# Performance work log

Hardware: AMD Instinct MI355X
Metric: run time of the kernel (lower is better)

The kernel has to match this reference:

```python
import jax, jax.numpy as jnp
import numpy as np

AMBIENT = [2, 2, 2]
DEGREES = [a + 1 for a in AMBIENT]          # coords per projective factor
N_COORDS = sum(DEGREES)                      # 9
STARTS = np.concatenate([[0], np.cumsum(DEGREES)[:-1]])
CONST_MULT = 1.0
CLIP = 1.0e6


def _get_real_imag_of_prod(cp):
    """cp: complex [B, n]. Returns (real [B, n(n+1)/2], imag [B, n(n-1)/2]).
    Matches TF boolean_mask(transpose(...)) ordering: row-major (b, a) with b<=a;
    real = (XX+YY)[x, b, a] (symmetric), imag = +XY_YX[x, b, a] for b<a."""
    X, Y = jnp.real(cp), jnp.imag(cp)
    XX_YY = jnp.einsum('xa,xb->xab', X, X) + jnp.einsum('xa,xb->xab', Y, Y)
    XY = jnp.einsum('xa,xb->xab', X, Y)
    XY_YX = XY - XY.transpose(0, 2, 1)      # antisymmetric
    n = cp.shape[1]
    iu = jnp.triu_indices(n)                # incl. diagonal
    su = jnp.triu_indices(n, 1)             # strict upper
    real = XX_YY[:, iu[0], iu[1]]
    imag = XY_YX[:, su[0], su[1]]
    return real, imag


def _bihom(points):
    """points: complex [B, N_COORDS] -> real [B, 729] section products / kappa."""
    B = points.shape[0]
    kappas_prod = jnp.ones((B,), points.real.dtype)
    it_r = it_i = None
    for i, (s, d) in enumerate(zip(STARTS, DEGREES)):
        cp = points[:, s:s + d]
        kappas_prod = kappas_prod * jnp.sum(jnp.abs(cp) ** 2, axis=-1)
        r, im = _get_real_imag_of_prod(cp)
        if i == 0:
            it_r, it_i = r, im
        else:
            new_r = jnp.concatenate([
                jnp.einsum('bi,bj->bij', it_r, r).reshape(B, -1),
                -jnp.einsum('bi,bj->bij', it_i, im).reshape(B, -1)], axis=1)
            new_i = jnp.concatenate([
                jnp.einsum('bi,bj->bij', it_r, im).reshape(B, -1),
                -jnp.einsum('bi,bj->bij', it_i, r).reshape(B, -1)], axis=1)
            it_r, it_i = new_r, new_i
    sec = jnp.concatenate([it_r, it_i], axis=-1)
    return sec / kappas_prod[:, None]


def _tower(h, W1, b1, W2, b2, W3, b3, Wf):
    # Dense layers with square activation, then log|.| into bias-free final Dense
    h = (h @ W1 + b1) ** 2
    h = (h @ W2 + b2) ** 2
    h = (h @ W3 + b3) ** 2
    return jnp.log(jnp.abs(h)) @ Wf


def setup_inputs() -> dict:
    key = jax.random.key(0)
    ks = jax.random.split(key, 16)
    B = 32768
    s = 0.05
    inp = {
        'x':   jax.random.normal(ks[0], (B, 2 * N_COORDS), jnp.float32),
        'W1a': jax.random.normal(ks[1], (729, 1024), jnp.float32) * s,
        'b1a': jax.random.normal(ks[2], (1024,), jnp.float32) * s,
        'W2a': jax.random.normal(ks[3], (1024, 1024), jnp.float32) * s,
        'b2a': jax.random.normal(ks[4], (1024,), jnp.float32) * s,
        'W3a': jax.random.normal(ks[5], (1024, 1), jnp.float32) * s,
        'b3a': jax.random.normal(ks[6], (1,), jnp.float32) * s,
        'Wfa': jnp.ones((1, 1), jnp.float32),
        'W1b': jax.random.normal(ks[7], (729, 1024), jnp.float32) * s,
        'b1b': jax.random.normal(ks[8], (1024,), jnp.float32) * s,
        'W2b': jax.random.normal(ks[9], (1024, 1024), jnp.float32) * s,
        'b2b': jax.random.normal(ks[10], (1024,), jnp.float32) * s,
        'W3b': jax.random.normal(ks[11], (1024, 1), jnp.float32) * s,
        'b3b': jax.random.normal(ks[12], (1,), jnp.float32) * s,
        'Wfb': jnp.ones((1, 1), jnp.float32),
    }
    return inp


def reference(x, W1a, b1a, W2a, b2a, W3a, b3a, Wfa,
              W1b, b1b, W2b, b2b, W3b, b3b, Wfb):
    points = jax.lax.complex(x[:, :N_COORDS], x[:, N_COORDS:])
    feats = _bihom(points)                     # [B, 729]
    out = _tower(feats, W1a, b1a, W2a, b2a, W3a, b3a, Wfa) \
        - _tower(feats, W1b, b1b, W2b, b2b, W3b, b3b, Wfb)
    return CONST_MULT * jnp.clip(out, -CLIP, CLIP)
```

## Files before the change

kernel.cpp:

```cpp
#include <hip/hip_runtime.h>

typedef unsigned short u16;
typedef unsigned int u32;
typedef __attribute__((ext_vector_type(8))) short bf16x8;
typedef __attribute__((ext_vector_type(4))) float f32x4;

__device__ __forceinline__ u16 f2bf(float x){
  unsigned u = __builtin_bit_cast(unsigned, x);
  unsigned r = (u + 0x7FFFu + ((u >> 16) & 1u)) >> 16;
  return (u16)r;
}
__device__ __forceinline__ float bf2f(u16 h){
  unsigned u = ((unsigned)h) << 16;
  return __builtin_bit_cast(float, u);
}

__device__ __forceinline__ void gld_lds16(const void* g, void* l){
  __builtin_amdgcn_global_load_lds((const __attribute__((address_space(1))) void*)g,
                                   (__attribute__((address_space(3))) void*)l,
                                   16, 0, 0);
}

__global__ void wconv_kernel(const float* __restrict__ W0, u16* __restrict__ Th0, int K0p,
                             const float* __restrict__ W1, u16* __restrict__ Th1, int K1p,
                             const float* __restrict__ W2, u16* __restrict__ Th2, int K2p,
                             const float* __restrict__ W3, u16* __restrict__ Th3, int K3p)
{
  __shared__ float t[32][33];
  int z = blockIdx.z;
  const float* W = z==0 ? W0 : z==1 ? W1 : z==2 ? W2 : W3;
  u16* Th = z==0 ? Th0 : z==1 ? Th1 : z==2 ? Th2 : Th3;
  int Kpad = z==0 ? K0p : z==1 ? K1p : z==2 ? K2p : K3p;
  int K = (Kpad == 768) ? 729 : 1024;
  int k0 = blockIdx.x * 32;
  if (k0 >= Kpad) return;
  int n0 = blockIdx.y * 32;
  int tx = threadIdx.x & 31, ty = threadIdx.x >> 5;
#pragma unroll
  for (int j = 0; j < 4; j++){
    int k = k0 + ty + j*8;
    float v = (k < K) ? W[(size_t)k*1024 + (n0 + tx)] : 0.f;
    t[ty + j*8][tx] = v;
  }
  __syncthreads();
#pragma unroll
  for (int j = 0; j < 4; j++){
    int n = n0 + ty + j*8;
    int k = k0 + tx;
    size_t idx = (size_t)n*Kpad + k;
    Th[idx] = f2bf(t[tx][ty + j*8]);
  }
}

__global__ void feats_kernel(const float* __restrict__ x,
                             u16* __restrict__ fh,
                             int row0)
{
  __shared__ float cC[8][28];
  __shared__ float tA[8][81];
  __shared__ float tB[8][12];
  __shared__ float ivk[8];
  const int tid = threadIdx.x;
  const int lrow0 = blockIdx.x * 8;
  if (tid < 8){
    const float* xr = x + (size_t)(row0 + lrow0 + tid) * 18;
    float kk = 1.f;
#pragma unroll
    for (int f = 0; f < 3; f++){
      float xa = xr[3*f+0], xb = xr[3*f+1], xc = xr[3*f+2];
      float ya = xr[9+3*f+0], yb = xr[9+3*f+1], yc = xr[9+3*f+2];
      int bse = f * 9;
      cC[tid][bse+0] = xa*xa + ya*ya;
      cC[tid][bse+1] = xa*xb + ya*yb;
      cC[tid][bse+2] = xa*xc + ya*yc;
      cC[tid][bse+3] = xb*xb + yb*yb;
      cC[tid][bse+4] = xb*xc + yb*yc;
      cC[tid][bse+5] = xc*xc + yc*yc;
      cC[tid][bse+6] = xa*yb - xb*ya;
      cC[tid][bse+7] = xa*yc - xc*ya;
      cC[tid][bse+8] = xb*yc - xc*yb;
      kk *= (xa*xa+ya*ya + xb*xb+yb*yb + xc*xc+yc*yc);
    }
    ivk[tid] = 1.f / kk;
#pragma unroll
    for (int j = 0; j < 6; j++) tB[tid][j] = cC[tid][18+j];
#pragma unroll
    for (int j = 0; j < 3; j++) tB[tid][6+j] = cC[tid][24+j];
  }
  __syncthreads();
#pragma unroll 1
  for (int e = tid; e < 648; e += 256){
    int r = e / 81;
    int k = e - r*81;
    const float* cc = cC[r];
    float val;
    if (k < 36)      {               val =   cc[k/6]     * cc[9  + k%6]; }
    else if (k < 45) { int u = k-36; val = -(cc[6 + u/3] * cc[15 + u%3]); }
    else if (k < 63) { int u = k-45; val =   cc[u/3]     * cc[15 + u%3]; }
    else             { int u = k-63; val = -(cc[6 + u/6] * cc[9  + u%6]); }
    tA[r][k] = val;
  }
  __syncthreads();
#pragma unroll 1
  for (int jj = 0; jj < 3; jj++){
    int o = jj*256 + tid;
    int idxA = 0, idxB = 0; float sgn = 0.f;
    if (o < 270)      {              idxA = o/6;      idxB = o - (o/6)*6; sgn =  1.f; }
    else if (o < 378) { int t = o-270; idxA = 45 + t/3; idxB = 6 + t%3;   sgn = -1.f; }
    else if (o < 513) { int t = o-378; idxA = t/3;      idxB = 6 + t%3;   sgn =  1.f; }
    else if (o < 729) { int t = o-513; idxA = 45 + t/6; idxB = t%6;       sgn = -1.f; }
#pragma unroll
    for (int r = 0; r < 8; r++){
      float v = sgn * tA[r][idxA] * tB[r][idxB] * ivk[r];
      size_t oi = (size_t)(lrow0 + r) * 768 + o;
      fh[oi] = f2bf(v);
    }
  }
}

#define GEMM_SMEM_BYTES (2*16384*2 + 4*256*4)

#define STAGE_A(BUF)  do{ u16* _a = sA + (BUF)*8192; \
    gld_lds16(gAh0, _a + wave*1024); gld_lds16(gAh1, _a + wave*1024 + 512); \
    gAh0 += 32; gAh1 += 32; }while(0)
#define STAGE_B(BUF) do{ u16* _b = sB + (BUF)*8192; \
    gld_lds16(gBh0, _b + wave*1024); gld_lds16(gBh1, _b + wave*1024 + 512); \
    gBh0 += 32; gBh1 += 32; }while(0)

#define BARRIER()  asm volatile("s_barrier" ::: "memory")
#define LGKM0()    asm volatile("s_waitcnt lgkmcnt(0)" ::: "memory")

#define CLUSTER(A, O, B) do{ \
    __builtin_amdgcn_s_setprio(1); \
    _Pragma("unroll") for (int m_ = 0; m_ < 4; m_++) \
      _Pragma("unroll") for (int n_ = 0; n_ < 4; n_++) \
        acc[(O)+m_][n_] = __builtin_amdgcn_mfma_f32_16x16x32_bf16((A)[m_], (B)[n_], acc[(O)+m_][n_], 0, 0, 0); \
    __builtin_amdgcn_s_setprio(0); \
  }while(0)

template<int MODE>
__global__ __launch_bounds__(512, 1) void gemm_k(
    const u16* __restrict__ Ahi,
    const u16* __restrict__ Bhi,
    const float* __restrict__ bias,
    u16* __restrict__ Oh,
    const float* __restrict__ W3, float* __restrict__ P, int Pstride,
    int K)
{
  extern __shared__ __align__(16) u16 smem[];
  u16* sA = smem;
  u16* sB = smem + 16384;
  float* rowsum = (float*)(smem + 32768);

  const int nwg = gridDim.x;
  const int qq = nwg >> 3;
  const int wg = (nwg & 7) ? (int)blockIdx.x
                           : ((blockIdx.x & 7) * qq + (blockIdx.x >> 3));
  const int nb = wg & 3;
  const int mb = wg >> 2;

  const int tid = threadIdx.x;
  const int wave = tid >> 6, lane = tid & 63;
  const int wm = wave >> 2, wn = wave & 3;

  const int l4 = lane >> 2, ls = lane & 3;
  const int fsw  = (l4 >> 1) & 3;
  const int koff = ((ls ^ fsw) << 3);

  const u16* gAh0 = Ahi + (size_t)(mb*256 + wave*32 + l4) * K + koff;
  const u16* gAh1 = gAh0 + (size_t)16 * K;
  const u16* gBh0 = Bhi + (size_t)(nb*256 + wave*32 + l4) * K + koff;
  const u16* gBh1 = gBh0 + (size_t)16 * K;

  const int r16 = lane & 15, g = lane >> 4;
  const int fr   = (r16 >> 1) & 3;
  const int slot = ((g ^ fr) << 3);

  f32x4 acc[8][4];
#pragma unroll
  for (int m = 0; m < 8; m++)
#pragma unroll
    for (int n = 0; n < 4; n++)
      acc[m][n] = (f32x4){0.f, 0.f, 0.f, 0.f};

  const int NT = K >> 5;
  STAGE_A(0); STAGE_B(0);
  asm volatile("s_waitcnt vmcnt(0)\n\ts_barrier" ::: "memory");

#pragma unroll 1
  for (int t = 0; t < NT; ++t){
    const int cur = t & 1, nxt = cur ^ 1;
    const u16* pA = sA + cur*8192;
    const u16* pB = sB + cur*8192;
    const bool pf = (t + 1 < NT);
    bf16x8 ah[8], bh[4];

#pragma unroll
    for (int n = 0; n < 4; n++) bh[n] = *(const bf16x8*)(pB + (wn*64 + n*16 + r16)*32 + slot);
#pragma unroll
    for (int m = 0; m < 4; m++) ah[m] = *(const bf16x8*)(pA + (wm*128 + m*16 + r16)*32 + slot);
    if (pf){ STAGE_A(nxt); }
    BARRIER(); LGKM0();
    CLUSTER(ah, 0, bh);
    BARRIER();

#pragma unroll
    for (int m = 0; m < 4; m++) ah[4+m] = *(const bf16x8*)(pA + (wm*128 + (4+m)*16 + r16)*32 + slot);
    if (pf){ STAGE_B(nxt); }
    BARRIER(); LGKM0();
    CLUSTER(ah+4, 4, bh);
    if (pf){
      asm volatile("s_waitcnt vmcnt(0)\n\ts_barrier" ::: "memory");
    } else {
      BARRIER();
    }
  }

  if constexpr (MODE == 0){
#pragma unroll
    for (int n = 0; n < 4; n++){
      int col = nb*256 + wn*64 + n*16 + r16;
      float bv = bias[col];
#pragma unroll
      for (int m = 0; m < 8; m++){
        int rbase = mb*256 + wm*128 + m*16 + g*4;
#pragma unroll
        for (int q = 0; q < 4; q++){
          float val = acc[m][n][q] + bv;
          val = val * val;
          size_t oi = (size_t)(rbase + q) * 1024 + col;
          Oh[oi] = f2bf(val);
        }
      }
    }
  } else {
    float w3v[4], bv[4];
#pragma unroll
    for (int n = 0; n < 4; n++){
      int col = nb*256 + wn*64 + n*16 + r16;
      w3v[n] = W3[col];
      bv[n]  = bias[col];
    }
    float rp[8][4];
#pragma unroll
    for (int m = 0; m < 8; m++)
#pragma unroll
      for (int q = 0; q < 4; q++)
        rp[m][q] = 0.f;
#pragma unroll
    for (int m = 0; m < 8; m++)
#pragma unroll
      for (int n = 0; n < 4; n++)
#pragma unroll
        for (int q = 0; q < 4; q++){
          float v = acc[m][n][q] + bv[n];
          rp[m][q] += v * v * w3v[n];
        }
#pragma unroll
    for (int m = 0; m < 8; m++)
#pragma unroll
      for (int q = 0; q < 4; q++){
        float s = rp[m][q];
        s += __shfl_xor(s, 1); s += __shfl_xor(s, 2);
        s += __shfl_xor(s, 4); s += __shfl_xor(s, 8);
        rp[m][q] = s;
      }
    if (r16 == 0){
#pragma unroll
      for (int m = 0; m < 8; m++)
#pragma unroll
        for (int q = 0; q < 4; q++)
          rowsum[wn*256 + wm*128 + m*16 + g*4 + q] = rp[m][q];
    }
    __syncthreads();
    if (tid < 256){
      float s = rowsum[tid] + rowsum[256 + tid] + rowsum[512 + tid] + rowsum[768 + tid];
      P[(size_t)nb * Pstride + mb*256 + tid] = s;
    }
  }
}

__global__ void finalize_kernel(const float* __restrict__ Pa, const float* __restrict__ Pb,
                                int Pstride,
                                const float* __restrict__ b3a, const float* __restrict__ Wfa,
                                const float* __restrict__ b3b, const float* __restrict__ Wfb,
                                float* __restrict__ out, int row0, int Rc)
{
  int r = blockIdx.x * 256 + threadIdx.x;
  if (r >= Rc) return;
  float sa = b3a[0], sb = b3b[0];
#pragma unroll
  for (int j = 0; j < 4; j++){
    sa += Pa[(size_t)j * Pstride + r];
    sb += Pb[(size_t)j * Pstride + r];
  }
  float ta = 2.f * logf(fabsf(sa)) * Wfa[0];
  float tb = 2.f * logf(fabsf(sb)) * Wfb[0];
  float o = ta - tb;
  o = fminf(fmaxf(o, -1000000.f), 1000000.f);
  out[row0 + r] = o;
}

static inline size_t align256(size_t v){ return (v + 255) & ~(size_t)255; }

extern "C" void kernel_launch(void* const* d_in, const int* in_sizes, int n_in,
                              void* d_out, int out_size, void* d_ws, size_t ws_size,
                              hipStream_t stream)
{
  (void)n_in; (void)out_size;
  const float* x   = (const float*)d_in[0];
  const float* W1a = (const float*)d_in[1];
  const float* b1a = (const float*)d_in[2];
  const float* W2a = (const float*)d_in[3];
  const float* b2a = (const float*)d_in[4];
  const float* W3a = (const float*)d_in[5];
  const float* b3a = (const float*)d_in[6];
  const float* Wfa = (const float*)d_in[7];
  const float* W1b = (const float*)d_in[8];
  const float* b1b = (const float*)d_in[9];
  const float* W2b = (const float*)d_in[10];
  const float* b2b = (const float*)d_in[11];
  const float* W3b = (const float*)d_in[12];
  const float* b3b = (const float*)d_in[13];
  const float* Wfb = (const float*)d_in[14];
  float* out = (float*)d_out;

  const int B  = in_sizes[0] / 18;
  const int K1 = 768;
  const int K2 = 1024;

  hipFuncSetAttribute((const void*)gemm_k<0>,
                      hipFuncAttributeMaxDynamicSharedMemorySize, GEMM_SMEM_BYTES);
  hipFuncSetAttribute((const void*)gemm_k<1>,
                      hipFuncAttributeMaxDynamicSharedMemorySize, GEMM_SMEM_BYTES);

  char* base = (char*)d_ws;
  size_t off = 0;
  auto carve = [&](size_t bytes) -> char* {
    off = align256(off);
    char* p = base + off;
    off += bytes;
    return p;
  };

  u16* wt1a = (u16*)carve((size_t)1024 * K1 * 2);
  u16* wt2a = (u16*)carve((size_t)1024 * K2 * 2);
  u16* wt1b = (u16*)carve((size_t)1024 * K1 * 2);
  u16* wt2b = (u16*)carve((size_t)1024 * K2 * 2);

  size_t fixed = align256(off);
  const long long per_row = (long long)K1*2 + 2048 + 32;
  long long avail = (long long)ws_size - (long long)fixed - 8192;
  long long rmax = avail > 0 ? avail / per_row : 0;
  int R = (int)((rmax / 256) * 256);
  if (R > B) R = B;
  if (R < 256) R = 256;

  u16* fh  = (u16*)carve((size_t)R * K1 * 2);
  u16* h1h = (u16*)carve((size_t)R * 1024 * 2);
  float* pa = (float*)carve((size_t)4 * R * 4);
  float* pb = (float*)carve((size_t)4 * R * 4);

  wconv_kernel<<<dim3(32, 32, 4), 256, 0, stream>>>(
      W1a, wt1a, K1,
      W2a, wt2a, K2,
      W1b, wt1b, K1,
      W2b, wt2b, K2);

  for (int row0 = 0; row0 < B; row0 += R){
    int Rc = B - row0; if (Rc > R) Rc = R;
    int MB = Rc / 256;
    feats_kernel<<<Rc/8, 256, 0, stream>>>(x, fh, row0);
    gemm_k<0><<<dim3(4*MB), 512, GEMM_SMEM_BYTES, stream>>>(
        fh, wt1a, b1a, h1h, nullptr, nullptr, 0, K1);
    gemm_k<1><<<dim3(4*MB), 512, GEMM_SMEM_BYTES, stream>>>(
        h1h, wt2a, b2a, nullptr, W3a, pa, R, K2);
    gemm_k<0><<<dim3(4*MB), 512, GEMM_SMEM_BYTES, stream>>>(
        fh, wt1b, b1b, h1h, nullptr, nullptr, 0, K1);
    gemm_k<1><<<dim3(4*MB), 512, GEMM_SMEM_BYTES, stream>>>(
        h1h, wt2b, b2b, nullptr, W3b, pb, R, K2);
    finalize_kernel<<<(Rc + 255)/256, 256, 0, stream>>>(pa, pb, R, b3a, Wfa, b3b, Wfb,
                                                        out, row0, Rc);
  }
}
```

Before: 308.5 us.

## Switch GEMM main loop to triple-buffered LDS with two-tile prefetch

Replaces the double-buffered, split A/B staging with barriers between two MFMA clusters by a three-stage LDS ring. Each iteration waits only for the oldest tile (vmcnt(4)), issues one barrier, prefetches the tile two steps ahead, then loads all fragments and runs all 32 MFMAs in one block. This gives global loads more latency cover and cuts barriers per iteration, at the cost of more LDS (about 100KB) and less interleaving of LDS reads with MFMA issue.

```diff
diff --git a/kernel.cpp b/kernel.cpp
--- a/kernel.cpp
+++ b/kernel.cpp
@@ -118,25 +118,16 @@
   }
 }
 
-#define GEMM_SMEM_BYTES (2*16384*2 + 4*256*4)
-
-#define STAGE_A(BUF)  do{ u16* _a = sA + (BUF)*8192; \
+#define GEMM_SMEM_BYTES (49152*2 + 4096)
+
+#define STAGE(BUF) do{ \
+    u16* _a = sA + (BUF)*8192; u16* _b = sB + (BUF)*8192; \
     gld_lds16(gAh0, _a + wave*1024); gld_lds16(gAh1, _a + wave*1024 + 512); \
-    gAh0 += 32; gAh1 += 32; }while(0)
-#define STAGE_B(BUF) do{ u16* _b = sB + (BUF)*8192; \
     gld_lds16(gBh0, _b + wave*1024); gld_lds16(gBh1, _b + wave*1024 + 512); \
-    gBh0 += 32; gBh1 += 32; }while(0)
+    gAh0 += 32; gAh1 += 32; gBh0 += 32; gBh1 += 32; \
+  }while(0)
 
 #define BARRIER()  asm volatile("s_barrier" ::: "memory")
-#define LGKM0()    asm volatile("s_waitcnt lgkmcnt(0)" ::: "memory")
-
-#define CLUSTER(A, O, B) do{ \
-    __builtin_amdgcn_s_setprio(1); \
-    _Pragma("unroll") for (int m_ = 0; m_ < 4; m_++) \
-      _Pragma("unroll") for (int n_ = 0; n_ < 4; n_++) \
-        acc[(O)+m_][n_] = __builtin_amdgcn_mfma_f32_16x16x32_bf16((A)[m_], (B)[n_], acc[(O)+m_][n_], 0, 0, 0); \
-    __builtin_amdgcn_s_setprio(0); \
-  }while(0)
 
 template<int MODE>
 __global__ __launch_bounds__(512, 1) void gemm_k(
@@ -149,8 +140,8 @@
 {
   extern __shared__ __align__(16) u16 smem[];
   u16* sA = smem;
-  u16* sB = smem + 16384;
-  float* rowsum = (float*)(smem + 32768);
+  u16* sB = smem + 24576;
+  float* rowsum = (float*)(smem + 49152);
 
   const int nwg = gridDim.x;
   const int qq = nwg >> 3;
@@ -184,36 +175,35 @@
       acc[m][n] = (f32x4){0.f, 0.f, 0.f, 0.f};
 
   const int NT = K >> 5;
-  STAGE_A(0); STAGE_B(0);
-  asm volatile("s_waitcnt vmcnt(0)\n\ts_barrier" ::: "memory");
+  STAGE(0); STAGE(1);
 
 #pragma unroll 1
   for (int t = 0; t < NT; ++t){
-    const int cur = t & 1, nxt = cur ^ 1;
+    if (t + 1 < NT){
+      asm volatile("s_waitcnt vmcnt(4)" ::: "memory");
+    } else {
+      asm volatile("s_waitcnt vmcnt(0)" ::: "memory");
+    }
+    BARRIER();
+    if (t + 2 < NT){
+      int b2 = (t + 2) % 3;
+      STAGE(b2);
+    }
+    const int cur = t % 3;
     const u16* pA = sA + cur*8192;
     const u16* pB = sB + cur*8192;
-    const bool pf = (t + 1 < NT);
     bf16x8 ah[8], bh[4];
-
 #pragma unroll
     for (int n = 0; n < 4; n++) bh[n] = *(const bf16x8*)(pB + (wn*64 + n*16 + r16)*32 + slot);
 #pragma unroll
-    for (int m = 0; m < 4; m++) ah[m] = *(const bf16x8*)(pA + (wm*128 + m*16 + r16)*32 + slot);
-    if (pf){ STAGE_A(nxt); }
-    BARRIER(); LGKM0();
-    CLUSTER(ah, 0, bh);
-    BARRIER();
-
-#pragma unroll
-    for (int m = 0; m < 4; m++) ah[4+m] = *(const bf16x8*)(pA + (wm*128 + (4+m)*16 + r16)*32 + slot);
-    if (pf){ STAGE_B(nxt); }
-    BARRIER(); LGKM0();
-    CLUSTER(ah+4, 4, bh);
-    if (pf){
-      asm volatile("s_waitcnt vmcnt(0)\n\ts_barrier" ::: "memory");
-    } else {
-      BARRIER();
-    }
+    for (int m = 0; m < 8; m++) ah[m] = *(const bf16x8*)(pA + (wm*128 + m*16 + r16)*32 + slot);
+    __builtin_amdgcn_s_setprio(1);
+#pragma unroll
+    for (int m = 0; m < 8; m++)
+#pragma unroll
+      for (int n = 0; n < 4; n++)
+        acc[m][n] = __builtin_amdgcn_mfma_f32_16x16x32_bf16(ah[m], bh[n], acc[m][n], 0, 0, 0);
+    __builtin_amdgcn_s_setprio(0);
   }
 
   if constexpr (MODE == 0){
```

New measurement: 285.6 us. 1.08x faster.
